# Performance work log

Measured on AMD Instinct MI355X. Metric: run time of the kernel, lower is better.

The kernel has to match this reference:

```python
import jax, jax.numpy as jnp
import numpy as np

VOCAB = 32000
EMB = 1024
SEQ = 2048
STACK = 8
N_HEADS = 16
ATTN = 64
BATCH = 2


def _ln(x, g, b, eps=1e-5):
    mu = jnp.mean(x, axis=-1, keepdims=True)
    var = jnp.var(x, axis=-1, keepdims=True)
    return (x - mu) * jax.lax.rsqrt(var + eps) * g + b


def setup_inputs() -> dict:
    key = jax.random.key(0)
    ks = jax.random.split(key, 16)
    s = lambda *sh: 0.02
    inp = {
        "x": jax.random.randint(ks[0], (BATCH, SEQ), 0, VOCAB),
        "emb": jax.random.normal(ks[1], (VOCAB, EMB), jnp.float32) * 0.02,
        # NOTE: one shared Attention_Head (all n_heads identical) and one shared Decoder (all stack layers identical)
        "Wq": jax.random.normal(ks[2], (EMB, ATTN), jnp.float32) * 0.02,
        "bq": jnp.zeros((ATTN,), jnp.float32),
        "Wk": jax.random.normal(ks[3], (EMB, ATTN), jnp.float32) * 0.02,
        "bk": jnp.zeros((ATTN,), jnp.float32),
        "Wv": jax.random.normal(ks[4], (EMB, ATTN), jnp.float32) * 0.02,
        "bv": jnp.zeros((ATTN,), jnp.float32),
        "Wd": jax.random.normal(ks[5], (ATTN * N_HEADS, EMB), jnp.float32) * 0.02,
        "bd": jnp.zeros((EMB,), jnp.float32),
        "g1": jnp.ones((EMB,), jnp.float32),
        "beta1": jnp.zeros((EMB,), jnp.float32),
        "g2": jnp.ones((EMB,), jnp.float32),
        "beta2": jnp.zeros((EMB,), jnp.float32),
        "W1": jax.random.normal(ks[6], (EMB, 4 * EMB), jnp.float32) * 0.02,
        "c1": jnp.zeros((4 * EMB,), jnp.float32),
        "W2": jax.random.normal(ks[7], (4 * EMB, EMB), jnp.float32) * 0.02,
        "c2": jnp.zeros((EMB,), jnp.float32),
        "Wfc": jax.random.normal(ks[8], (EMB, VOCAB), jnp.float32) * 0.02,
        "bfc": jnp.zeros((VOCAB,), jnp.float32),
    }
    return inp


def reference(x, emb, Wq, bq, Wk, bk, Wv, bv, Wd, bd, g1, beta1, g2, beta2, W1, c1, W2, c2, Wfc, bfc):
    h = emb[x]  # [B, S, E]
    scale = ATTN ** (-0.5)
    for _ in range(STACK):  # same (shared) decoder params every layer
        z = _ln(h, g1, beta1)
        q = z @ Wq + bq  # [B,S,A]
        k = z @ Wk + bk
        v = z @ Wv + bv
        # no causal mask applied in the original (tril buffer is unused)
        attn = jax.nn.softmax(jnp.einsum("bqa,bka->bqk", q, k) * scale, axis=-1)
        head = attn @ v  # [B,S,A]; all heads share weights -> identical outputs
        cat = jnp.tile(head, (1, 1, N_HEADS))  # [B,S,A*H]
        h = h + cat @ Wd + bd
        z2 = _ln(h, g2, beta2)
        h = h + jax.nn.relu(z2 @ W1 + c1) @ W2 + c2
    return h @ Wfc + bfc  # [B,S,VOCAB]
```

## Files before the change

### kernel.cpp

```cpp
#include <hip/hip_runtime.h>

typedef unsigned short u16;
typedef __attribute__((ext_vector_type(4))) float f32x4;
typedef __attribute__((ext_vector_type(8))) __bf16 bf16x8;
typedef __attribute__((ext_vector_type(4))) unsigned short u16x4;

static __device__ __forceinline__ u16 f2bf(float f) {
  union { float f; unsigned u; } v; v.f = f;
  unsigned r = v.u + 0x7fffu + ((v.u >> 16) & 1u);
  return (u16)(r >> 16);
}

#define GLD_LDS(g, l) __builtin_amdgcn_global_load_lds( \
    (const __attribute__((address_space(1))) void*)(g), \
    (__attribute__((address_space(3))) void*)(l), 16, 0, 0)

template<int EPI>
__global__ __launch_bounds__(512, 2)
void gemm8p(const u16* __restrict__ A, const u16* __restrict__ B,
            float* __restrict__ Cf, u16* __restrict__ Cb,
            const float* __restrict__ bias, float alpha,
            int K, int lda, int ldb, int ldc, int mtiles, int gm, int nsplit,
            long long sA, long long sB, long long sC)
{
  extern __shared__ u16 lds8[];
  const int t = threadIdx.x;
  const int w = t >> 6, l = t & 63;
  const int l15 = l & 15, l16 = l >> 4;
  const int wr = w >> 2, wc = w & 3;

  int wg = blockIdx.x;
  const int nwg = gridDim.x;
  {
    const int q = nwg >> 3, r = nwg & 7;
    const int xcd = wg & 7, loc = wg >> 3;
    wg = (xcd < r ? xcd * (q + 1) : r * (q + 1) + (xcd - r) * q) + loc;
  }
  const int ntiles = nwg / mtiles;
  const int gsz = gm * ntiles;
  const int gi = wg / gsz;
  const int rr = wg - gi * gsz;
  const int nt = rr / gm;
  const int mt = gi * gm + (rr - nt * gm);
  const int m0 = mt << 8, n0 = nt << 8;

  const int bz = blockIdx.z;
  int batch = bz, sp = 0;
  if (nsplit > 1) { batch = bz / nsplit; sp = bz - batch * nsplit; }
  const u16* Ab = A + (long long)batch * sA + (long long)sp * K;
  const u16* Bb = B + (long long)batch * sB + (long long)sp * K;
  const long long cbase = (long long)bz * sC;

  const int srow = t >> 3;
  const int scol = (((t & 7) ^ (srow & 7)) << 3);
  const u16* gA[4]; const u16* gB[4];
#pragma unroll
  for (int i = 0; i < 4; ++i) {
    gA[i] = Ab + (long long)(m0 + i * 64 + srow) * lda + scol;
    gB[i] = Bb + (long long)(n0 + i * 64 + srow) * ldb + scol;
  }
  const int ldst = w << 9;

  auto STAGE = [&](int buf) {
#pragma unroll
    for (int i = 0; i < 4; ++i) {
      GLD_LDS(gA[i], &lds8[buf * 16384 + i * 4096 + ldst]);
      gA[i] += 64;
    }
#pragma unroll
    for (int i = 0; i < 4; ++i) {
      GLD_LDS(gB[i], &lds8[32768 + buf * 16384 + i * 4096 + ldst]);
      gB[i] += 64;
    }
  };

  STAGE(0);
  STAGE(1);

  f32x4 acc[8][4] = {};
  const int nkt = K >> 6;
  const int aRow = wr * 128 + l15;
  const int bRow = wc * 64 + l15;
  const int swz = l15 & 7;

  for (int kt = 0; kt < nkt; ++kt) {
    const int buf = kt & 1;
    if (kt < nkt - 1) asm volatile("s_waitcnt vmcnt(8)" ::: "memory");
    else              asm volatile("s_waitcnt vmcnt(0)" ::: "memory");
    __builtin_amdgcn_s_barrier();
    __builtin_amdgcn_sched_barrier(0);

    const int abase = buf * 16384;
    const int bbase = 32768 + buf * 16384;
    bf16x8 af[4][2], bf[4][2];
#pragma unroll
    for (int mf = 0; mf < 4; ++mf)
#pragma unroll
      for (int kk = 0; kk < 2; ++kk)
        af[mf][kk] = *(const bf16x8*)&lds8[abase + (aRow + mf * 16) * 64 + ((((kk << 2) + l16)) ^ swz) * 8];
#pragma unroll
    for (int nf = 0; nf < 4; ++nf)
#pragma unroll
      for (int kk = 0; kk < 2; ++kk)
        bf[nf][kk] = *(const bf16x8*)&lds8[bbase + (bRow + nf * 16) * 64 + ((((kk << 2) + l16)) ^ swz) * 8];

    __builtin_amdgcn_s_setprio(1);
#pragma unroll
    for (int mf = 0; mf < 4; ++mf)
#pragma unroll
      for (int nf = 0; nf < 4; ++nf)
#pragma unroll
        for (int kk = 0; kk < 2; ++kk)
          acc[mf][nf] = __builtin_amdgcn_mfma_f32_16x16x32_bf16(af[mf][kk], bf[nf][kk], acc[mf][nf], 0, 0, 0);
    __builtin_amdgcn_s_setprio(0);

    bf16x8 ah[4][2];
#pragma unroll
    for (int mf = 0; mf < 4; ++mf)
#pragma unroll
      for (int kk = 0; kk < 2; ++kk)
        ah[mf][kk] = *(const bf16x8*)&lds8[abase + (aRow + 64 + mf * 16) * 64 + ((((kk << 2) + l16)) ^ swz) * 8];

    asm volatile("s_waitcnt lgkmcnt(0)" ::: "memory");
    __builtin_amdgcn_s_barrier();
    __builtin_amdgcn_sched_barrier(0);
    if (kt + 2 < nkt) STAGE(buf);

    __builtin_amdgcn_s_setprio(1);
#pragma unroll
    for (int mf = 0; mf < 4; ++mf)
#pragma unroll
      for (int nf = 0; nf < 4; ++nf)
#pragma unroll
        for (int kk = 0; kk < 2; ++kk)
          acc[mf + 4][nf] = __builtin_amdgcn_mfma_f32_16x16x32_bf16(ah[mf][kk], bf[nf][kk], acc[mf + 4][nf], 0, 0, 0);
    __builtin_amdgcn_s_setprio(0);
  }

#pragma unroll
  for (int mf = 0; mf < 8; ++mf) {
    const int rbase = m0 + wr * 128 + mf * 16 + l16 * 4;
#pragma unroll
    for (int nf = 0; nf < 4; ++nf) {
      const int col = n0 + wc * 64 + nf * 16 + l15;
      const float bv = bias ? bias[col] : 0.f;
#pragma unroll
      for (int r = 0; r < 4; ++r) {
        const long long idx = cbase + (long long)(rbase + r) * ldc + col;
        const float v = acc[mf][nf][r];
        if (EPI == 0)      Cf[idx] = alpha * v + bv;
        else if (EPI == 2) Cb[idx] = f2bf(v + bv);
        else               { float x = v + bv; Cb[idx] = f2bf(x > 0.f ? x : 0.f); }
      }
    }
  }
}

template<int EPI>
__global__ __launch_bounds__(256)
void gemm_bt(const u16* __restrict__ A, const u16* __restrict__ B,
             float* __restrict__ Cf, u16* __restrict__ Cb,
             const float* __restrict__ bias, float alpha,
             int K, int lda, int ldb, int ldc, int mtiles, int gm, int nsplit,
             long long sA, long long sB, long long sC)
{
  __shared__ u16 ldsA[128 * 32];
  __shared__ u16 ldsB[128 * 32];
  const int t = threadIdx.x;
  const int w = t >> 6, l = t & 63;

  int wg = blockIdx.x;
  const int nwg = gridDim.x;
  {
    const int q = nwg >> 3, r = nwg & 7;
    const int xcd = wg & 7, loc = wg >> 3;
    wg = (xcd < r ? xcd * (q + 1) : r * (q + 1) + (xcd - r) * q) + loc;
  }
  const int ntiles = nwg / mtiles;
  const int gsz = gm * ntiles;
  const int gi = wg / gsz;
  const int rr = wg - gi * gsz;
  const int nt = rr / gm;
  const int mt = gi * gm + (rr - nt * gm);
  const int m0 = mt << 7, n0 = nt << 7;

  const int bzRaw = blockIdx.z;
  int batch = bzRaw, sp = 0;
  if (nsplit > 1) { batch = bzRaw / nsplit; sp = bzRaw - batch * nsplit; }
  const u16* Ab = A + (long long)batch * sA + (long long)sp * K;
  const u16* Bb = B + (long long)batch * sB + (long long)sp * K;
  const long long cbase = (long long)bzRaw * sC;

  const int wr = (w >> 1) << 6, wc = (w & 1) << 6;
  const int l15 = l & 15, l16 = l >> 4;
  f32x4 acc[4][4] = {};

  for (int k0 = 0; k0 < K; k0 += 32) {
#pragma unroll
    for (int r = 0; r < 2; ++r) {
      const int o = (r << 12) + (t << 4);
      const int row = o >> 6;
      const int cole = (o & 63) >> 1;
      GLD_LDS(Ab + (long long)(m0 + row) * lda + k0 + cole, &ldsA[(r << 11) + (w << 9)]);
      GLD_LDS(Bb + (long long)(n0 + row) * ldb + k0 + cole, &ldsB[(r << 11) + (w << 9)]);
    }
    __syncthreads();
    bf16x8 af[4], bg[4];
#pragma unroll
    for (int i = 0; i < 4; ++i) {
      af[i] = *(const bf16x8*)&ldsA[(wr + i * 16 + l15) * 32 + l16 * 8];
      bg[i] = *(const bf16x8*)&ldsB[(wc + i * 16 + l15) * 32 + l16 * 8];
    }
#pragma unroll
    for (int i = 0; i < 4; ++i)
#pragma unroll
      for (int j = 0; j < 4; ++j)
        acc[i][j] = __builtin_amdgcn_mfma_f32_16x16x32_bf16(af[i], bg[j], acc[i][j], 0, 0, 0);
    __syncthreads();
  }

#pragma unroll
  for (int i = 0; i < 4; ++i) {
    const int rbase = m0 + wr + i * 16 + l16 * 4;
#pragma unroll
    for (int j = 0; j < 4; ++j) {
      const int col = n0 + wc + j * 16 + l15;
      const float bv = bias ? bias[col] : 0.f;
#pragma unroll
      for (int r = 0; r < 4; ++r) {
        const long long idx = cbase + (long long)(rbase + r) * ldc + col;
        const float v = acc[i][j][r];
        if (EPI == 0)      Cf[idx] = alpha * v + bv;
        else if (EPI == 1) Cf[idx] += v + bv;
        else if (EPI == 2) Cb[idx] = f2bf(v + bv);
        else               { float x = v + bv; Cb[idx] = f2bf(x > 0.f ? x : 0.f); }
      }
    }
  }
}

__device__ __forceinline__ void fstep(
    const bf16x8 (&ck)[4][2], const bf16x8 (&cv)[4][2],
    bf16x8 (&nk)[4][2], bf16x8 (&nv)[4][2],
    const bf16x8 (&qf)[2], float (&m)[4], float (&ls)[4], f32x4 (&o)[4],
    const u16* qb, const u16* vb, int kvn, u16* pl, int l15, int l16)
{
  f32x4 s[4] = {};
#pragma unroll
  for (int ni = 0; ni < 4; ++ni)
#pragma unroll
    for (int kk = 0; kk < 2; ++kk)
      s[ni] = __builtin_amdgcn_mfma_f32_16x16x32_bf16(qf[kk], ck[ni][kk], s[ni], 0, 0, 0);
#pragma unroll
  for (int ni = 0; ni < 4; ++ni)
#pragma unroll
    for (int kk = 0; kk < 2; ++kk)
      nk[ni][kk] = *(const bf16x8*)(qb + (kvn + ni * 16 + l15) * 256 + 64 + kk * 32 + l16 * 8);
#pragma unroll
  for (int ni = 0; ni < 4; ++ni) s[ni] *= 0.125f;
  float al[4], ps[4];
#pragma unroll
  for (int r = 0; r < 4; ++r) {
    float v = fmaxf(fmaxf(s[0][r], s[1][r]), fmaxf(s[2][r], s[3][r]));
    v = fmaxf(v, __shfl_xor(v, 1)); v = fmaxf(v, __shfl_xor(v, 2));
    v = fmaxf(v, __shfl_xor(v, 4)); v = fmaxf(v, __shfl_xor(v, 8));
    const float mn = fmaxf(m[r], v);
    al[r] = __expf(m[r] - mn);
    m[r] = mn;
    ps[r] = 0.f;
  }
#pragma unroll
  for (int ni = 0; ni < 4; ++ni)
#pragma unroll
    for (int r = 0; r < 4; ++r) {
      const float p = __expf(s[ni][r] - m[r]);
      ps[r] += p;
      pl[(l16 * 4 + r) * 72 + ni * 16 + l15] = f2bf(p);
    }
#pragma unroll
  for (int r = 0; r < 4; ++r) {
    float t = ps[r];
    t += __shfl_xor(t, 1); t += __shfl_xor(t, 2);
    t += __shfl_xor(t, 4); t += __shfl_xor(t, 8);
    ls[r] = ls[r] * al[r] + t;
  }
#pragma unroll
  for (int nd = 0; nd < 4; ++nd)
#pragma unroll
    for (int r = 0; r < 4; ++r) o[nd][r] *= al[r];
  bf16x8 pa[2];
#pragma unroll
  for (int kk = 0; kk < 2; ++kk)
    pa[kk] = *(const bf16x8*)&pl[l15 * 72 + kk * 32 + l16 * 8];
#pragma unroll
  for (int nd = 0; nd < 4; ++nd)
#pragma unroll
    for (int kk = 0; kk < 2; ++kk)
      o[nd] = __builtin_amdgcn_mfma_f32_16x16x32_bf16(pa[kk], cv[nd][kk], o[nd], 0, 0, 0);
#pragma unroll
  for (int nd = 0; nd < 4; ++nd)
#pragma unroll
    for (int kk = 0; kk < 2; ++kk)
      nv[nd][kk] = *(const bf16x8*)(vb + (nd * 16 + l15) * 2048 + kvn + kk * 32 + l16 * 8);
}

__global__ __launch_bounds__(64)
void flashp_k(const u16* __restrict__ qkv, const u16* __restrict__ vT,
              float* __restrict__ po, float* __restrict__ pm, float* __restrict__ pls)
{
  __shared__ u16 pl[16 * 72];
  const int l = threadIdx.x, l15 = l & 15, l16 = l >> 4;
  const int idx = blockIdx.x;
  const int b = idx >> 9, rest = idx & 511, sp = rest >> 7, qt = rest & 127;
  const int q0 = qt << 4, kvb = sp << 9;
  const u16* qb = qkv + (long long)b * 2048 * 256;
  const u16* vb = vT + (long long)b * 64 * 2048;
  bf16x8 qf[2];
#pragma unroll
  for (int kk = 0; kk < 2; ++kk)
    qf[kk] = *(const bf16x8*)(qb + (q0 + l15) * 256 + kk * 32 + l16 * 8);
  float m[4], ls[4];
  f32x4 o[4] = {};
#pragma unroll
  for (int r = 0; r < 4; ++r) { m[r] = -1e30f; ls[r] = 0.f; }
  bf16x8 ka[4][2], va[4][2], kb[4][2], vb2[4][2];
#pragma unroll
  for (int ni = 0; ni < 4; ++ni)
#pragma unroll
    for (int kk = 0; kk < 2; ++kk) {
      ka[ni][kk] = *(const bf16x8*)(qb + (kvb + ni * 16 + l15) * 256 + 64 + kk * 32 + l16 * 8);
      va[ni][kk] = *(const bf16x8*)(vb + (ni * 16 + l15) * 2048 + kvb + kk * 32 + l16 * 8);
    }
  for (int ti = 0; ti < 8; ti += 2) {
    const int n1 = kvb + (ti + 1 < 8 ? (ti + 1) * 64 : 7 * 64);
    const int n2 = kvb + (ti + 2 < 8 ? (ti + 2) * 64 : 7 * 64);
    fstep(ka, va, kb, vb2, qf, m, ls, o, qb, vb, n1, pl, l15, l16);
    fstep(kb, vb2, ka, va, qf, m, ls, o, qb, vb, n2, pl, l15, l16);
  }
  const long long pidx = ((long long)(b * 128 + qt)) * 4 + sp;
#pragma unroll
  for (int nd = 0; nd < 4; ++nd)
#pragma unroll
    for (int r = 0; r < 4; ++r)
      po[pidx * 1024 + (l16 * 4 + r) * 64 + nd * 16 + l15] = o[nd][r];
  if (l15 == 0) {
#pragma unroll
    for (int r = 0; r < 4; ++r) {
      pm[pidx * 16 + l16 * 4 + r] = m[r];
      pls[pidx * 16 + l16 * 4 + r] = ls[r];
    }
  }
}

__global__ __launch_bounds__(64)
void fmerge_k(const float* __restrict__ po, const float* __restrict__ pm,
              const float* __restrict__ pls, u16* __restrict__ head)
{
  const int idx = blockIdx.x;
  const int d = threadIdx.x;
  const long long base = (long long)idx * 4;
#pragma unroll
  for (int r = 0; r < 16; ++r) {
    float M = -1e30f;
#pragma unroll
    for (int sp = 0; sp < 4; ++sp) M = fmaxf(M, pm[(base + sp) * 16 + r]);
    float L = 0.f, acc = 0.f;
#pragma unroll
    for (int sp = 0; sp < 4; ++sp) {
      const float e = __expf(pm[(base + sp) * 16 + r] - M);
      L += pls[(base + sp) * 16 + r] * e;
      acc += po[(base + sp) * 1024 + r * 64 + d] * e;
    }
    head[((long long)idx * 16 + r) * 64 + d] = f2bf(acc / L);
  }
}

__global__ __launch_bounds__(256)
void ln_k(const float* __restrict__ x, const float* __restrict__ g,
          const float* __restrict__ b, u16* __restrict__ z)
{
  const long long row = blockIdx.x;
  f32x4 v = ((const f32x4*)(x + row * 1024))[threadIdx.x];
  float s = v[0] + v[1] + v[2] + v[3];
  float q = v[0] * v[0] + v[1] * v[1] + v[2] * v[2] + v[3] * v[3];
#pragma unroll
  for (int o = 32; o; o >>= 1) { s += __shfl_down(s, o); q += __shfl_down(q, o); }
  __shared__ float rs_[4], rq_[4];
  const int l = threadIdx.x & 63, w = threadIdx.x >> 6;
  if (l == 0) { rs_[w] = s; rq_[w] = q; }
  __syncthreads();
  s = rs_[0] + rs_[1] + rs_[2] + rs_[3];
  q = rq_[0] + rq_[1] + rq_[2] + rq_[3];
  const float mu = s * (1.f / 1024.f);
  const float rstd = rsqrtf(q * (1.f / 1024.f) - mu * mu + 1e-5f);
  const f32x4 gv = ((const f32x4*)g)[threadIdx.x];
  const f32x4 bv = ((const f32x4*)b)[threadIdx.x];
  u16x4 o4;
#pragma unroll
  for (int e = 0; e < 4; ++e) o4[e] = f2bf((v[e] - mu) * rstd * gv[e] + bv[e]);
  ((u16x4*)(z + row * 1024))[threadIdx.x] = o4;
}

template<int MODE>
__global__ __launch_bounds__(256)
void reduce_ln_k(const u16* __restrict__ p, float* __restrict__ h,
                 const float* __restrict__ c2, const float* __restrict__ g,
                 const float* __restrict__ b, u16* __restrict__ z)
{
  const long long row = blockIdx.x;
  const int t = threadIdx.x;
  const long long i4 = (row << 8) + t;
  f32x4 v = ((const f32x4*)h)[i4] + ((const f32x4*)c2)[t];
#pragma unroll
  for (int s = 0; s < 4; ++s) {
    u16x4 pv = ((const u16x4*)p)[i4 + (long long)s * 1048576];
#pragma unroll
    for (int e = 0; e < 4; ++e) {
      union { unsigned u; float f; } x; x.u = ((unsigned)pv[e]) << 16;
      v[e] += x.f;
    }
  }
  u16x4 o4;
  if (MODE == 1) {
#pragma unroll
    for (int e = 0; e < 4; ++e) o4[e] = f2bf(v[e]);
  } else {
    ((f32x4*)h)[i4] = v;
    float s = v[0] + v[1] + v[2] + v[3];
    float q = v[0] * v[0] + v[1] * v[1] + v[2] * v[2] + v[3] * v[3];
#pragma unroll
    for (int o = 32; o; o >>= 1) { s += __shfl_down(s, o); q += __shfl_down(q, o); }
    __shared__ float rs_[4], rq_[4];
    const int l = t & 63, w = t >> 6;
    if (l == 0) { rs_[w] = s; rq_[w] = q; }
    __syncthreads();
    s = rs_[0] + rs_[1] + rs_[2] + rs_[3];
    q = rq_[0] + rq_[1] + rq_[2] + rq_[3];
    const float mu = s * (1.f / 1024.f);
    const float rstd = rsqrtf(q * (1.f / 1024.f) - mu * mu + 1e-5f);
    const f32x4 gv = ((const f32x4*)g)[t];
    const f32x4 bv = ((const f32x4*)b)[t];
#pragma unroll
    for (int e = 0; e < 4; ++e) o4[e] = f2bf((v[e] - mu) * rstd * gv[e] + bv[e]);
  }
  ((u16x4*)z)[i4] = o4;
}

__global__ __launch_bounds__(256)
void gather_k(const int* __restrict__ x, const float* __restrict__ emb, float* __restrict__ h)
{
  const long long tok = blockIdx.x;
  const long long r = (long long)x[tok] << 8;
  ((f32x4*)h)[(tok << 8) + threadIdx.x] = ((const f32x4*)emb)[r + threadIdx.x];
}

__global__ __launch_bounds__(256)
void tcast_k(const float* __restrict__ in, u16* __restrict__ out, int R, int C)
{
  __shared__ float tile[32][33];
  const int tx = threadIdx.x & 31, ty = threadIdx.x >> 5;
  const long long r0 = (long long)blockIdx.y << 5, c0 = (long long)blockIdx.x << 5;
#pragma unroll
  for (int yy = 0; yy < 32; yy += 8)
    tile[ty + yy][tx] = in[(r0 + ty + yy) * C + c0 + tx];
  __syncthreads();
#pragma unroll
  for (int yy = 0; yy < 32; yy += 8)
    out[(c0 + ty + yy) * R + r0 + tx] = f2bf(tile[tx][ty + yy]);
}

__global__ __launch_bounds__(256)
void wqkv_k(const float* __restrict__ Wq, const float* __restrict__ Wk,
            const float* __restrict__ Wv, u16* __restrict__ o)
{
  const int n = blockIdx.y;
  const long long e = (long long)blockIdx.x * 256 + threadIdx.x;
  float v = 0.f;
  if (n < 64)       v = Wq[e * 64 + n];
  else if (n < 128) v = Wk[e * 64 + (n - 64)];
  else if (n < 192) v = Wv[e * 64 + (n - 128)];
  o[(long long)n * 1024 + e] = f2bf(v);
}

__global__ __launch_bounds__(256)
void bqkv_k(const float* __restrict__ bq, const float* __restrict__ bk,
            const float* __restrict__ bv, float* __restrict__ o)
{
  const int n = threadIdx.x;
  float v = 0.f;
  if (n < 64)       v = bq[n];
  else if (n < 128) v = bk[n - 64];
  else if (n < 192) v = bv[n - 128];
  o[n] = v;
}

__global__ __launch_bounds__(256)
void wdsum_k(const float* __restrict__ Wd, u16* __restrict__ o)
{
  const int i = blockIdx.x * 256 + threadIdx.x;
  const int a = i & 63, e = i >> 6;
  float s = 0.f;
#pragma unroll
  for (int hh = 0; hh < 16; ++hh) s += Wd[(long long)(hh * 64 + a) * 1024 + e];
  o[i] = f2bf(s);
}

__global__ __launch_bounds__(256)
void reduce_qkv(const float* __restrict__ p, const float* __restrict__ bqkv,
                u16* __restrict__ qkv, u16* __restrict__ vT)
{
  const long long i4 = (long long)blockIdx.x * 256 + threadIdx.x;
  const int c4 = (int)(i4 & 63);
  const long long row = i4 >> 6;
  f32x4 s = ((const f32x4*)p)[i4] + ((const f32x4*)p)[i4 + 262144]
          + ((const f32x4*)bqkv)[c4];
  u16x4 o;
#pragma unroll
  for (int e = 0; e < 4; ++e) o[e] = f2bf(s[e]);
  ((u16x4*)qkv)[i4] = o;
  if (c4 >= 32 && c4 < 48) {
    const long long b = row >> 11, sidx = row & 2047;
#pragma unroll
    for (int e = 0; e < 4; ++e) {
      const int a = (c4 - 32) * 4 + e;
      vT[(b * 64 + a) * 2048 + sidx] = o[e];
    }
  }
}

extern "C" void kernel_launch(void* const* d_in, const int* in_sizes, int n_in,
                              void* d_out, int out_size, void* d_ws, size_t ws_size,
                              hipStream_t stream) {
  const int*   x   = (const int*)d_in[0];
  const float* emb = (const float*)d_in[1];
  const float* Wq  = (const float*)d_in[2];
  const float* bq  = (const float*)d_in[3];
  const float* Wk  = (const float*)d_in[4];
  const float* bk  = (const float*)d_in[5];
  const float* Wv  = (const float*)d_in[6];
  const float* bv  = (const float*)d_in[7];
  const float* Wd  = (const float*)d_in[8];
  const float* bd  = (const float*)d_in[9];
  const float* g1  = (const float*)d_in[10];
  const float* be1 = (const float*)d_in[11];
  const float* g2  = (const float*)d_in[12];
  const float* be2 = (const float*)d_in[13];
  const float* W1  = (const float*)d_in[14];
  const float* c1  = (const float*)d_in[15];
  const float* W2  = (const float*)d_in[16];
  const float* c2  = (const float*)d_in[17];
  const float* Wfc = (const float*)d_in[18];
  const float* bfc = (const float*)d_in[19];
  float* out = (float*)d_out;

  hipFuncSetAttribute(reinterpret_cast<const void*>(gemm8p<0>),
                      hipFuncAttributeMaxDynamicSharedMemorySize, 131072);
  hipFuncSetAttribute(reinterpret_cast<const void*>(gemm8p<2>),
                      hipFuncAttributeMaxDynamicSharedMemorySize, 131072);
  hipFuncSetAttribute(reinterpret_cast<const void*>(gemm8p<3>),
                      hipFuncAttributeMaxDynamicSharedMemorySize, 131072);

  char* ws = (char*)d_ws;
  size_t off = 0;
  auto alloc = [&](size_t bytes) { void* p = ws + off; off = (off + bytes + 255) & ~(size_t)255; return p; };
  float*  h     = (float*) alloc(4096ull * 1024 * 4);
  u16*    z     = (u16*)   alloc(4096ull * 1024 * 2);
  u16*    qkv   = (u16*)   alloc(4096ull * 256 * 2);
  u16*    vT    = (u16*)   alloc(2ull * 64 * 2048 * 2);
  u16*    head  = (u16*)   alloc(4096ull * 64 * 2);
  u16*    mid   = (u16*)   alloc(4096ull * 4096 * 2);
  char*   SCR   = (char*)  alloc(2ull * 4096 * 1024 * 4);
  float*  partQ = (float*)SCR;
  float*  po    = (float*)SCR;
  float*  pm    = (float*)(SCR + 4194304);
  float*  pls   = (float*)(SCR + 4194304 + 65536);
  u16*    partF = (u16*)SCR;
  u16*    Wqkvt = (u16*)   alloc(256ull * 1024 * 2);
  float*  bqkv  = (float*) alloc(256 * 4);
  u16*    Wdst  = (u16*)   alloc(1024ull * 64 * 2);
  u16*    W1t   = (u16*)   alloc(4096ull * 1024 * 2);
  u16*    W2t   = (u16*)   alloc(1024ull * 4096 * 2);
  u16*    Wfct  = (u16*)   alloc(32000ull * 1024 * 2);

  gather_k<<<4096, 256, 0, stream>>>(x, emb, h);
  wqkv_k<<<dim3(4, 256), 256, 0, stream>>>(Wq, Wk, Wv, Wqkvt);
  bqkv_k<<<1, 256, 0, stream>>>(bq, bk, bv, bqkv);
  wdsum_k<<<256, 256, 0, stream>>>(Wd, Wdst);
  tcast_k<<<dim3(128, 32), 256, 0, stream>>>(W1, W1t, 1024, 4096);
  tcast_k<<<dim3(32, 128), 256, 0, stream>>>(W2, W2t, 4096, 1024);
  tcast_k<<<dim3(1000, 32), 256, 0, stream>>>(Wfc, Wfct, 1024, 32000);

  for (int layer = 0; layer < 8; ++layer) {
    if (layer == 0)
      ln_k<<<4096, 256, 0, stream>>>(h, g1, be1, z);
    gemm_bt<0><<<dim3(64, 1, 2), 256, 0, stream>>>(z, Wqkvt, partQ, nullptr, nullptr, 1.f,
        512, 1024, 1024, 256, 32, 32, 2, 0, 0, 1048576);
    reduce_qkv<<<1024, 256, 0, stream>>>(partQ, bqkv, qkv, vT);
    flashp_k<<<1024, 64, 0, stream>>>(qkv, vT, po, pm, pls);
    fmerge_k<<<256, 64, 0, stream>>>(po, pm, pls, head);
    gemm_bt<1><<<dim3(256, 1, 1), 256, 0, stream>>>(head, Wdst, h, nullptr, bd, 1.f,
        64, 64, 64, 1024, 32, 32, 1, 0, 0, 0);
    ln_k<<<4096, 256, 0, stream>>>(h, g2, be2, z);
    gemm8p<3><<<dim3(256, 1, 1), 512, 131072, stream>>>(z, W1t, nullptr, mid, c1, 1.f,
        1024, 1024, 1024, 4096, 16, 16, 1, 0, 0, 0);
    gemm8p<2><<<dim3(64, 1, 4), 512, 131072, stream>>>(mid, W2t, nullptr, partF, nullptr, 1.f,
        1024, 4096, 4096, 1024, 16, 16, 4, 0, 0, 4194304);
    if (layer < 7)
      reduce_ln_k<0><<<4096, 256, 0, stream>>>(partF, h, c2, g1, be1, z);
    else
      reduce_ln_k<1><<<4096, 256, 0, stream>>>(partF, h, c2, nullptr, nullptr, z);
  }
  gemm8p<0><<<dim3(2000, 1, 1), 512, 131072, stream>>>(z, Wfct, out, nullptr, bfc, 1.f,
      1024, 1024, 1024, 32000, 16, 8, 1, 0, 0, 0);
}
```

Measured before the change: 1.807 ms.

## Fuse flash split-K merge into attention block and fuse Wd GEMM with LayerNorm

```diff
diff --git a/kernel.cpp b/kernel.cpp
--- a/kernel.cpp
+++ b/kernel.cpp
@@ -304,17 +304,20 @@
       nv[nd][kk] = *(const bf16x8*)(vb + (nd * 16 + l15) * 2048 + kvn + kk * 32 + l16 * 8);
 }
 
-__global__ __launch_bounds__(64)
-void flashp_k(const u16* __restrict__ qkv, const u16* __restrict__ vT,
-              float* __restrict__ po, float* __restrict__ pm, float* __restrict__ pls)
-{
-  __shared__ u16 pl[16 * 72];
-  const int l = threadIdx.x, l15 = l & 15, l16 = l >> 4;
-  const int idx = blockIdx.x;
-  const int b = idx >> 9, rest = idx & 511, sp = rest >> 7, qt = rest & 127;
-  const int q0 = qt << 4, kvb = sp << 9;
+__global__ __launch_bounds__(256)
+void flash4_k(const u16* __restrict__ qkv, const u16* __restrict__ vT,
+              u16* __restrict__ head)
+{
+  __shared__ u16 plbuf[4][16 * 72];
+  __shared__ float poL[4][16][64];
+  __shared__ float pmL[4][16], plsL[4][16];
+  const int t = threadIdx.x, sp = t >> 6, l = t & 63;
+  const int l15 = l & 15, l16 = l >> 4;
+  const int b = blockIdx.x >> 7, q0 = (blockIdx.x & 127) << 4;
+  const int kvb = sp << 9;
   const u16* qb = qkv + (long long)b * 2048 * 256;
   const u16* vb = vT + (long long)b * 64 * 2048;
+  u16* pl = &plbuf[sp][0];
   bf16x8 qf[2];
 #pragma unroll
   for (int kk = 0; kk < 2; ++kk)
@@ -337,41 +340,105 @@
     fstep(ka, va, kb, vb2, qf, m, ls, o, qb, vb, n1, pl, l15, l16);
     fstep(kb, vb2, ka, va, qf, m, ls, o, qb, vb, n2, pl, l15, l16);
   }
-  const long long pidx = ((long long)(b * 128 + qt)) * 4 + sp;
 #pragma unroll
   for (int nd = 0; nd < 4; ++nd)
 #pragma unroll
     for (int r = 0; r < 4; ++r)
-      po[pidx * 1024 + (l16 * 4 + r) * 64 + nd * 16 + l15] = o[nd][r];
+      poL[sp][l16 * 4 + r][nd * 16 + l15] = o[nd][r];
   if (l15 == 0) {
 #pragma unroll
     for (int r = 0; r < 4; ++r) {
-      pm[pidx * 16 + l16 * 4 + r] = m[r];
-      pls[pidx * 16 + l16 * 4 + r] = ls[r];
-    }
-  }
-}
-
-__global__ __launch_bounds__(64)
-void fmerge_k(const float* __restrict__ po, const float* __restrict__ pm,
-              const float* __restrict__ pls, u16* __restrict__ head)
-{
-  const int idx = blockIdx.x;
-  const int d = threadIdx.x;
-  const long long base = (long long)idx * 4;
-#pragma unroll
-  for (int r = 0; r < 16; ++r) {
-    float M = -1e30f;
-#pragma unroll
-    for (int sp = 0; sp < 4; ++sp) M = fmaxf(M, pm[(base + sp) * 16 + r]);
+      pmL[sp][l16 * 4 + r] = m[r];
+      plsL[sp][l16 * 4 + r] = ls[r];
+    }
+  }
+  __syncthreads();
+#pragma unroll
+  for (int i = 0; i < 4; ++i) {
+    const int oi = t + i * 256;
+    const int row = oi >> 6, col = oi & 63;
+    float M = fmaxf(fmaxf(pmL[0][row], pmL[1][row]), fmaxf(pmL[2][row], pmL[3][row]));
     float L = 0.f, acc = 0.f;
 #pragma unroll
-    for (int sp = 0; sp < 4; ++sp) {
-      const float e = __expf(pm[(base + sp) * 16 + r] - M);
-      L += pls[(base + sp) * 16 + r] * e;
-      acc += po[(base + sp) * 1024 + r * 64 + d] * e;
-    }
-    head[((long long)idx * 16 + r) * 64 + d] = f2bf(acc / L);
+    for (int s2 = 0; s2 < 4; ++s2) {
+      const float e = __expf(pmL[s2][row] - M);
+      L += plsL[s2][row] * e;
+      acc += poL[s2][row][col] * e;
+    }
+    head[((long long)b * 2048 + q0 + row) * 64 + col] = f2bf(acc / L);
+  }
+}
+
+__global__ __launch_bounds__(256)
+void hwd_ln_k(const u16* __restrict__ head, const u16* __restrict__ Wdst,
+              const float* __restrict__ bd, float* __restrict__ h,
+              const float* __restrict__ g, const float* __restrict__ be,
+              u16* __restrict__ z)
+{
+  const int t = threadIdx.x, w = t >> 6, l = t & 63;
+  const int l15 = l & 15, l16 = l >> 4;
+  const int r0 = blockIdx.x << 4;
+  const int c0 = w << 8;
+  bf16x8 af[2];
+#pragma unroll
+  for (int kk = 0; kk < 2; ++kk)
+    af[kk] = *(const bf16x8*)&head[(long long)(r0 + l15) * 64 + kk * 32 + l16 * 8];
+  f32x4 acc[16];
+#pragma unroll
+  for (int nf = 0; nf < 16; ++nf) {
+    const int e = c0 + nf * 16 + l15;
+    f32x4 a = {0.f, 0.f, 0.f, 0.f};
+    bf16x8 b0 = *(const bf16x8*)&Wdst[e * 64 + l16 * 8];
+    bf16x8 b1 = *(const bf16x8*)&Wdst[e * 64 + 32 + l16 * 8];
+    a = __builtin_amdgcn_mfma_f32_16x16x32_bf16(af[0], b0, a, 0, 0, 0);
+    a = __builtin_amdgcn_mfma_f32_16x16x32_bf16(af[1], b1, a, 0, 0, 0);
+    acc[nf] = a;
+  }
+  float ps[4] = {0.f, 0.f, 0.f, 0.f}, pq[4] = {0.f, 0.f, 0.f, 0.f};
+#pragma unroll
+  for (int nf = 0; nf < 16; ++nf) {
+    const int col = c0 + nf * 16 + l15;
+#pragma unroll
+    for (int r = 0; r < 4; ++r) {
+      const long long row = r0 + l16 * 4 + r;
+      float v = h[row * 1024 + col] + acc[nf][r] + bd[col];
+      acc[nf][r] = v;
+      ps[r] += v; pq[r] += v * v;
+    }
+  }
+#pragma unroll
+  for (int r = 0; r < 4; ++r) {
+#pragma unroll
+    for (int msk = 1; msk < 16; msk <<= 1) {
+      ps[r] += __shfl_xor(ps[r], msk);
+      pq[r] += __shfl_xor(pq[r], msk);
+    }
+  }
+  __shared__ float S[4][16], Q[4][16];
+  if (l15 == 0) {
+#pragma unroll
+    for (int r = 0; r < 4; ++r) { S[w][l16 * 4 + r] = ps[r]; Q[w][l16 * 4 + r] = pq[r]; }
+  }
+  __syncthreads();
+  float mu[4], rstd[4];
+#pragma unroll
+  for (int r = 0; r < 4; ++r) {
+    const int ri = l16 * 4 + r;
+    const float s = S[0][ri] + S[1][ri] + S[2][ri] + S[3][ri];
+    const float q = Q[0][ri] + Q[1][ri] + Q[2][ri] + Q[3][ri];
+    mu[r] = s * (1.f / 1024.f);
+    rstd[r] = rsqrtf(q * (1.f / 1024.f) - mu[r] * mu[r] + 1e-5f);
+  }
+#pragma unroll
+  for (int nf = 0; nf < 16; ++nf) {
+    const int col = c0 + nf * 16 + l15;
+    const float gc = g[col], bc = be[col];
+#pragma unroll
+    for (int r = 0; r < 4; ++r) {
+      const long long row = r0 + l16 * 4 + r;
+      h[row * 1024 + col] = acc[nf][r];
+      z[row * 1024 + col] = f2bf((acc[nf][r] - mu[r]) * rstd[r] * gc + bc);
+    }
   }
 }
 
@@ -571,9 +638,6 @@
   u16*    mid   = (u16*)   alloc(4096ull * 4096 * 2);
   char*   SCR   = (char*)  alloc(2ull * 4096 * 1024 * 4);
   float*  partQ = (float*)SCR;
-  float*  po    = (float*)SCR;
-  float*  pm    = (float*)(SCR + 4194304);
-  float*  pls   = (float*)(SCR + 4194304 + 65536);
   u16*    partF = (u16*)SCR;
   u16*    Wqkvt = (u16*)   alloc(256ull * 1024 * 2);
   float*  bqkv  = (float*) alloc(256 * 4);
@@ -596,11 +660,8 @@
     gemm_bt<0><<<dim3(64, 1, 2), 256, 0, stream>>>(z, Wqkvt, partQ, nullptr, nullptr, 1.f,
         512, 1024, 1024, 256, 32, 32, 2, 0, 0, 1048576);
     reduce_qkv<<<1024, 256, 0, stream>>>(partQ, bqkv, qkv, vT);
-    flashp_k<<<1024, 64, 0, stream>>>(qkv, vT, po, pm, pls);
-    fmerge_k<<<256, 64, 0, stream>>>(po, pm, pls, head);
-    gemm_bt<1><<<dim3(256, 1, 1), 256, 0, stream>>>(head, Wdst, h, nullptr, bd, 1.f,
-        64, 64, 64, 1024, 32, 32, 1, 0, 0, 0);
-    ln_k<<<4096, 256, 0, stream>>>(h, g2, be2, z);
+    flash4_k<<<256, 256, 0, stream>>>(qkv, vT, head);
+    hwd_ln_k<<<256, 256, 0, stream>>>(head, Wdst, bd, h, g2, be2, z);
     gemm8p<3><<<dim3(256, 1, 1), 512, 131072, stream>>>(z, W1t, nullptr, mid, c1, 1.f,
         1024, 1024, 1024, 4096, 16, 16, 1, 0, 0, 0);
     gemm8p<2><<<dim3(64, 1, 4), 512, 131072, stream>>>(mid, W2t, nullptr, partF, nullptr, 1.f,
```

New measurement: 1.557 ms. -13.8%, faster.
